# Performance work log

Hardware: AMD Instinct MI355X
Metric: run time of the kernel (lower is better)

The kernel has to match this reference:

```python
import jax, jax.numpy as jnp
import numpy as np

N_NODES = 50000
N_EDGES = 800000
N_GRAPHS = 128
IN_DIM, HID_DIM, OUT_DIM = 128, 96, 10


def setup_inputs() -> dict:
    key = jax.random.key(0)
    ks = jax.random.split(key, 9)
    x = jax.random.normal(ks[0], (N_NODES, IN_DIM), dtype=jnp.float32)
    edge_index = jax.random.randint(ks[1], (2, N_EDGES), 0, N_NODES, dtype=jnp.int32)
    batch = jnp.sort(jax.random.randint(ks[2], (N_NODES,), 0, N_GRAPHS, dtype=jnp.int32))
    s1 = 1.0 / np.sqrt(IN_DIM)
    s2 = 1.0 / np.sqrt(HID_DIM)
    W1 = jax.random.uniform(ks[3], (IN_DIM, HID_DIM), jnp.float32, -s1, s1)
    b1 = jnp.zeros((HID_DIM,), jnp.float32)
    W2 = jax.random.uniform(ks[4], (HID_DIM, HID_DIM), jnp.float32, -s2, s2)
    b2 = jnp.zeros((HID_DIM,), jnp.float32)
    Wf = jax.random.uniform(ks[5], (OUT_DIM, HID_DIM), jnp.float32, -s2, s2)
    bf = jax.random.uniform(ks[6], (OUT_DIM,), jnp.float32, -s2, s2)
    return {"x": x, "edge_index": edge_index, "batch": batch,
            "W1": W1, "b1": b1, "W2": W2, "b2": b2, "Wf": Wf, "bf": bf}


def reference(x, edge_index, batch, W1, b1, W2, b2, Wf, bf):
    n = x.shape[0]
    row, col = edge_index[0], edge_index[1]
    # GCN symmetric normalization with self-loops: deg = 1 + in-degree
    deg = jax.ops.segment_sum(jnp.ones_like(col, dtype=x.dtype), col, num_segments=n) + 1.0
    dinv = deg ** -0.5  # [N]
    norm = dinv[row] * dinv[col]  # [E]

    def gcn_conv(h, W, b):
        h = h @ W  # [N, F_out]
        # edge messages: norm_e * h[src] scattered to dst; self-loops handled analytically
        agg = jax.ops.segment_sum(norm[:, None] * h[row], col, num_segments=n)
        agg = agg + (dinv * dinv)[:, None] * h
        return agg + b

    h = jax.nn.relu(gcn_conv(x, W1, b1))
    h = gcn_conv(h, W2, b2)

    # global mean pool over graphs
    counts = jax.ops.segment_sum(jnp.ones((n,), x.dtype), batch, num_segments=N_GRAPHS)
    pooled = jax.ops.segment_sum(h, batch, num_segments=N_GRAPHS)
    pooled = pooled / jnp.maximum(counts, 1.0)[:, None]

    logits = pooled @ Wf.T + bf
    return jax.nn.log_softmax(logits, axis=1)
```

## Files before the change

kernel.cpp:

```cpp
#include <hip/hip_runtime.h>
#include <hip/hip_bf16.h>

#define N_GRAPHS 128
#define HID 96
#define OUT_DIM 10
#define CAP 64

typedef __attribute__((ext_vector_type(8))) short short8;
typedef __attribute__((ext_vector_type(4))) float f32x4;
typedef __attribute__((ext_vector_type(2))) float f32x2;

__device__ inline unsigned short f2bf(float f) {
    union { float f; unsigned u; } x;
    x.f = f;
    unsigned r = x.u + 0x7FFFu + ((x.u >> 16) & 1u);
    return (unsigned short)(r >> 16);
}

__device__ inline unsigned char f2fp8(float v) {
    int p = __builtin_amdgcn_cvt_pk_fp8_f32(v, v, 0, false);
    return (unsigned char)(p & 0xff);
}

__device__ inline void unpack16_fp8(uint4 v, float* o) {
    f32x2 a0 = __builtin_amdgcn_cvt_pk_f32_fp8((int)v.x, false);
    f32x2 a1 = __builtin_amdgcn_cvt_pk_f32_fp8((int)v.x, true);
    f32x2 b0 = __builtin_amdgcn_cvt_pk_f32_fp8((int)v.y, false);
    f32x2 b1 = __builtin_amdgcn_cvt_pk_f32_fp8((int)v.y, true);
    f32x2 c0 = __builtin_amdgcn_cvt_pk_f32_fp8((int)v.z, false);
    f32x2 c1 = __builtin_amdgcn_cvt_pk_f32_fp8((int)v.z, true);
    f32x2 d0 = __builtin_amdgcn_cvt_pk_f32_fp8((int)v.w, false);
    f32x2 d1 = __builtin_amdgcn_cvt_pk_f32_fp8((int)v.w, true);
    o[0] = a0.x;  o[1] = a0.y;  o[2] = a1.x;  o[3] = a1.y;
    o[4] = b0.x;  o[5] = b0.y;  o[6] = b1.x;  o[7] = b1.y;
    o[8] = c0.x;  o[9] = c0.y;  o[10] = c1.x; o[11] = c1.y;
    o[12] = d0.x; o[13] = d0.y; o[14] = d1.x; o[15] = d1.y;
}

__global__ __launch_bounds__(256) void fill_kernel(const int* __restrict__ rowi,
                                                   const int* __restrict__ coli,
                                                   int* __restrict__ cnt,
                                                   unsigned short* __restrict__ srcs,
                                                   int E, int N) {
    const int part = blockIdx.x & 7;
    const int chunk = blockIdx.x >> 3;
    const int base = chunk * 2048;
    const int plo = (int)(((long long)N * part) >> 3);
    const int phi = (int)(((long long)N * (part + 1)) >> 3);
#pragma unroll
    for (int it = 0; it < 8; ++it) {
        int e = base + it * 256 + threadIdx.x;
        if (e < E) {
            int c = coli[e];
            if (c >= plo && c < phi) {
                int pos = atomicAdd(&cnt[c], 1);
                if (pos < CAP) srcs[(size_t)c * CAP + pos] = (unsigned short)rowi[e];
            }
        }
    }
}

__global__ __launch_bounds__(256) void gemm1_mfma(const float* __restrict__ X,
                                                  const float* __restrict__ W,
                                                  const int* __restrict__ cnt,
                                                  unsigned char* __restrict__ Tp, int N) {
    constexpr int K = 128;
    constexpr int P = K + 8;
    constexpr int KT = K / 32;
    __shared__ __align__(16) unsigned short Wt[96 * P];
    const int tid = threadIdx.x;
    const int row0 = blockIdx.x * 64;

    for (int idx = tid; idx < K * 96; idx += 256) {
        int k = idx / 96, n = idx - k * 96;
        Wt[n * P + k] = f2bf(W[idx]);
    }
    __syncthreads();

    const int wv = tid >> 6;
    const int lane = tid & 63;
    const int m = lane & 15;
    const int quad = lane >> 4;
    const int row = row0 + wv * 16 + m;

    short8 afrag[KT];
    if (row < N) {
        const float* Xr = X + (size_t)row * K;
#pragma unroll
        for (int t = 0; t < KT; ++t) {
            float4 a0 = *(const float4*)(Xr + t * 32 + quad * 8);
            float4 a1 = *(const float4*)(Xr + t * 32 + quad * 8 + 4);
            short8 a;
            a[0] = (short)f2bf(a0.x); a[1] = (short)f2bf(a0.y);
            a[2] = (short)f2bf(a0.z); a[3] = (short)f2bf(a0.w);
            a[4] = (short)f2bf(a1.x); a[5] = (short)f2bf(a1.y);
            a[6] = (short)f2bf(a1.z); a[7] = (short)f2bf(a1.w);
            afrag[t] = a;
        }
    } else {
#pragma unroll
        for (int t = 0; t < KT; ++t) afrag[t] = short8{0, 0, 0, 0, 0, 0, 0, 0};
    }

    f32x4 acc[6];
#pragma unroll
    for (int nt = 0; nt < 6; ++nt) acc[nt] = f32x4{0.f, 0.f, 0.f, 0.f};
#pragma unroll
    for (int t = 0; t < KT; ++t) {
#pragma unroll
        for (int nt = 0; nt < 6; ++nt) {
            short8 bfrag = *(const short8*)&Wt[(nt * 16 + m) * P + t * 32 + quad * 8];
            acc[nt] = __builtin_amdgcn_mfma_f32_16x16x32_bf16(afrag[t], bfrag, acc[nt], 0, 0, 0);
        }
    }
#pragma unroll
    for (int r = 0; r < 4; ++r) {
        int orow = row0 + wv * 16 + quad * 4 + r;
        if (orow < N) {
            float d = rsqrtf(1.0f + (float)cnt[orow]);
#pragma unroll
            for (int nt = 0; nt < 6; ++nt)
                Tp[(size_t)orow * 96 + nt * 16 + m] = f2fp8(d * acc[nt][r]);
        }
    }
}

__global__ __launch_bounds__(256) void gather1_gemm2(const unsigned char* __restrict__ Tp1,
                                                     const unsigned short* __restrict__ srcs,
                                                     const int* __restrict__ cnt,
                                                     const float* __restrict__ b1,
                                                     const float* __restrict__ W2,
                                                     unsigned char* __restrict__ Tp2, int N) {
    constexpr int PH = 104;
    constexpr int PW = 104;
    __shared__ __align__(16) unsigned short Hs[128 * PH];
    __shared__ __align__(16) unsigned short Wt[96 * PW];
    const int tid = threadIdx.x;
    const int node0 = blockIdx.x * 128;

    for (int idx = tid; idx < 96 * 96; idx += 256) {
        int k = idx / 96, n = idx - k * 96;
        Wt[n * PW + k] = f2bf(W2[idx]);
    }

    const uint4* Trow = (const uint4*)Tp1;
#pragma unroll
    for (int it = 0; it < 3; ++it) {
        int idx = it * 256 + tid;
        int n = idx / 6, j = idx - n * 6;
        int i = node0 + n;
        if (i < N) {
            float acc[16], tmp[16];
            unpack16_fp8(Trow[(size_t)i * 6 + j], acc);
            int ci = cnt[i];
            int e = min(ci, CAP);
            const unsigned short* sp = srcs + (size_t)i * CAP;
            int k = 0;
            for (; k + 4 <= e; k += 4) {
                ushort4 s4 = *(const ushort4*)(sp + k);
                uint4 v0 = Trow[(size_t)s4.x * 6 + j];
                uint4 v1 = Trow[(size_t)s4.y * 6 + j];
                uint4 v2 = Trow[(size_t)s4.z * 6 + j];
                uint4 v3 = Trow[(size_t)s4.w * 6 + j];
                unpack16_fp8(v0, tmp);
#pragma unroll
                for (int l = 0; l < 16; ++l) acc[l] += tmp[l];
                unpack16_fp8(v1, tmp);
#pragma unroll
                for (int l = 0; l < 16; ++l) acc[l] += tmp[l];
                unpack16_fp8(v2, tmp);
#pragma unroll
                for (int l = 0; l < 16; ++l) acc[l] += tmp[l];
                unpack16_fp8(v3, tmp);
#pragma unroll
                for (int l = 0; l < 16; ++l) acc[l] += tmp[l];
            }
            for (; k < e; ++k) {
                unpack16_fp8(Trow[(size_t)sp[k] * 6 + j], tmp);
#pragma unroll
                for (int l = 0; l < 16; ++l) acc[l] += tmp[l];
            }
            float di = rsqrtf(1.0f + (float)ci);
#pragma unroll
            for (int l = 0; l < 16; ++l) {
                float v = fmaxf(di * acc[l] + b1[j * 16 + l], 0.0f);
                Hs[n * PH + j * 16 + l] = f2bf(v);
            }
        } else {
#pragma unroll
            for (int l = 0; l < 16; ++l) Hs[n * PH + j * 16 + l] = 0;
        }
    }
    __syncthreads();

    const int wv = tid >> 6;
    const int lane = tid & 63;
    const int m = lane & 15;
    const int quad = lane >> 4;
#pragma unroll
    for (int half = 0; half < 2; ++half) {
        const int rt = wv + half * 4;
        const int lrow = rt * 16 + m;
        short8 afrag[3];
#pragma unroll
        for (int t = 0; t < 3; ++t)
            afrag[t] = *(const short8*)&Hs[lrow * PH + t * 32 + quad * 8];
        f32x4 acc[6];
#pragma unroll
        for (int nt = 0; nt < 6; ++nt) acc[nt] = f32x4{0.f, 0.f, 0.f, 0.f};
#pragma unroll
        for (int t = 0; t < 3; ++t) {
#pragma unroll
            for (int nt = 0; nt < 6; ++nt) {
                short8 bfrag = *(const short8*)&Wt[(nt * 16 + m) * PW + t * 32 + quad * 8];
                acc[nt] = __builtin_amdgcn_mfma_f32_16x16x32_bf16(afrag[t], bfrag, acc[nt], 0, 0, 0);
            }
        }
#pragma unroll
        for (int r = 0; r < 4; ++r) {
            int orow = node0 + rt * 16 + quad * 4 + r;
            if (orow < N) {
                float d = rsqrtf(1.0f + (float)cnt[orow]);
#pragma unroll
                for (int nt = 0; nt < 6; ++nt)
                    Tp2[(size_t)orow * 96 + nt * 16 + m] = f2fp8(d * acc[nt][r]);
            }
        }
    }
}

__global__ __launch_bounds__(192) void gather2_pool(const unsigned char* __restrict__ Tp,
                                                    const unsigned short* __restrict__ srcs,
                                                    const int* __restrict__ cnt,
                                                    const int* __restrict__ batch,
                                                    float* __restrict__ pooled, int N) {
    __shared__ float hl[32 * 96];
    __shared__ int g_l[32];
    const int tid = threadIdx.x;
    const int n = tid / 6;
    const int j = tid - n * 6;
    const int i = blockIdx.x * 32 + n;
    if (tid < 32) {
        int ii = blockIdx.x * 32 + tid;
        g_l[tid] = (ii < N) ? batch[ii] : -1;
    }

    float acc[16];
#pragma unroll
    for (int l = 0; l < 16; ++l) acc[l] = 0.0f;
    float di = 0.0f;
    if (i < N) {
        const uint4* Trow = (const uint4*)Tp;
        float tmp[16];
        unpack16_fp8(Trow[(size_t)i * 6 + j], acc);
        int ci = cnt[i];
        di = rsqrtf(1.0f + (float)ci);
        int e = min(ci, CAP);
        const unsigned short* sp = srcs + (size_t)i * CAP;
        int k = 0;
        for (; k + 4 <= e; k += 4) {
            ushort4 s4 = *(const ushort4*)(sp + k);
            uint4 v0 = Trow[(size_t)s4.x * 6 + j];
            uint4 v1 = Trow[(size_t)s4.y * 6 + j];
            uint4 v2 = Trow[(size_t)s4.z * 6 + j];
            uint4 v3 = Trow[(size_t)s4.w * 6 + j];
            unpack16_fp8(v0, tmp);
#pragma unroll
            for (int l = 0; l < 16; ++l) acc[l] += tmp[l];
            unpack16_fp8(v1, tmp);
#pragma unroll
            for (int l = 0; l < 16; ++l) acc[l] += tmp[l];
            unpack16_fp8(v2, tmp);
#pragma unroll
            for (int l = 0; l < 16; ++l) acc[l] += tmp[l];
            unpack16_fp8(v3, tmp);
#pragma unroll
            for (int l = 0; l < 16; ++l) acc[l] += tmp[l];
        }
        for (; k < e; ++k) {
            unpack16_fp8(Trow[(size_t)sp[k] * 6 + j], tmp);
#pragma unroll
            for (int l = 0; l < 16; ++l) acc[l] += tmp[l];
        }
    }
#pragma unroll
    for (int l = 0; l < 16; ++l) hl[n * 96 + j * 16 + l] = di * acc[l];
    __syncthreads();

    if (tid < 96) {
        int f = tid;
        float s = 0.0f;
        int gcur = -2;
        for (int nn = 0; nn < 32; ++nn) {
            int g = g_l[nn];
            if (g < 0) continue;
            if (g != gcur) {
                if (gcur >= 0) atomicAdd(&pooled[gcur * 96 + f], s);
                gcur = g;
                s = 0.0f;
            }
            s += hl[nn * 96 + f];
        }
        if (gcur >= 0) atomicAdd(&pooled[gcur * 96 + f], s);
    }
}

__device__ inline int lower_bound_dev(const int* __restrict__ a, int n, int val) {
    int lo = 0, hi = n;
    while (lo < hi) {
        int m = (lo + hi) >> 1;
        if (a[m] < val) lo = m + 1; else hi = m;
    }
    return lo;
}

__global__ void head_kernel(const float* __restrict__ pooled, const int* __restrict__ batch,
                            const float* __restrict__ b2, const float* __restrict__ Wf,
                            const float* __restrict__ bfv, float* __restrict__ out, int N) {
    __shared__ float wfs[OUT_DIM * HID];
    __shared__ float b2s[HID];
    __shared__ float bfs[OUT_DIM];
    int t = threadIdx.x;
    for (int idx = t; idx < OUT_DIM * HID; idx += 128) wfs[idx] = Wf[idx];
    if (t < HID) b2s[t] = b2[t];
    if (t < OUT_DIM) bfs[t] = bfv[t];
    __syncthreads();
    int g = t;
    if (g >= N_GRAPHS) return;
    int lo = lower_bound_dev(batch, N, g);
    int hi = lower_bound_dev(batch, N, g + 1);
    int c = hi - lo;
    float inv = (c > 0) ? 1.0f / (float)c : 0.0f;
    float hasb = (c > 0) ? 1.0f : 0.0f;
    float logits[OUT_DIM];
#pragma unroll
    for (int o = 0; o < OUT_DIM; ++o) {
        float s = 0.0f;
        for (int cc = 0; cc < HID; ++cc)
            s += (pooled[g * HID + cc] * inv + hasb * b2s[cc]) * wfs[o * HID + cc];
        logits[o] = s + bfs[o];
    }
    float m = logits[0];
#pragma unroll
    for (int o = 1; o < OUT_DIM; ++o) m = fmaxf(m, logits[o]);
    float se = 0.0f;
#pragma unroll
    for (int o = 0; o < OUT_DIM; ++o) se += expf(logits[o] - m);
    float lse = m + logf(se);
#pragma unroll
    for (int o = 0; o < OUT_DIM; ++o) out[g * OUT_DIM + o] = logits[o] - lse;
}

extern "C" void kernel_launch(void* const* d_in, const int* in_sizes, int n_in,
                              void* d_out, int out_size, void* d_ws, size_t ws_size,
                              hipStream_t stream) {
    const float* x     = (const float*)d_in[0];
    const int*   ei    = (const int*)d_in[1];
    const int*   batch = (const int*)d_in[2];
    const float* W1    = (const float*)d_in[3];
    const float* b1    = (const float*)d_in[4];
    const float* W2    = (const float*)d_in[5];
    const float* b2    = (const float*)d_in[6];
    const float* Wf    = (const float*)d_in[7];
    const float* bf    = (const float*)d_in[8];

    const int N = in_sizes[0] / 128;
    const int E = in_sizes[1] / 2;
    const int* rowi = ei;
    const int* coli = ei + E;

    size_t off = 0;
    auto alloc = [&](size_t bytes) {
        void* p = (char*)d_ws + off;
        off += (bytes + 255) & ~(size_t)255;
        return p;
    };
    int*            cnt    = (int*)alloc((size_t)N * 4);
    float*          pooled = (float*)alloc((size_t)N_GRAPHS * HID * 4);
    size_t zero_bytes = off;
    unsigned short* srcs   = (unsigned short*)alloc((size_t)N * CAP * 2);
    unsigned char*  Tp1    = (unsigned char*)alloc((size_t)N * HID);
    unsigned char*  Tp2    = (unsigned char*)alloc((size_t)N * HID);

    hipMemsetAsync(d_ws, 0, zero_bytes, stream);

    const int nchunk = (E + 2047) / 2048;
    fill_kernel<<<nchunk * 8, 256, 0, stream>>>(rowi, coli, cnt, srcs, E, N);

    gemm1_mfma<<<(N + 63) / 64, 256, 0, stream>>>(x, W1, cnt, Tp1, N);

    gather1_gemm2<<<(N + 127) / 128, 256, 0, stream>>>(Tp1, srcs, cnt, b1, W2, Tp2, N);

    gather2_pool<<<(N + 31) / 32, 192, 0, stream>>>(Tp2, srcs, cnt, batch, pooled, N);

    head_kernel<<<1, 128, 0, stream>>>(pooled, batch, b2, Wf, bf, (float*)d_out, N);
}
```

Measured before the change: 215.2 us.

## Pad fp8 feature rows to 128 bytes, halve gather tile, count graph sizes via atomics

Feature tables Tp1 and Tp2 now use a 128-byte row stride instead of 96, so every gathered row starts on a cache-line boundary and addressing becomes a shift. gather1_gemm2 processes 64 nodes per block instead of 128, which raises the block count and shrinks shared memory per block. Per-graph node counts are now accumulated with atomics inside fill_kernel, replacing the binary searches in the single-block head kernel. The padding costs extra memory footprint, and the per-node atomics add some contention.

Measured after the change: 319.1 us. 48.2% more time.

```diff
diff --git a/kernel.cpp b/kernel.cpp
--- a/kernel.cpp
+++ b/kernel.cpp
@@ -5,6 +5,7 @@
 #define HID 96
 #define OUT_DIM 10
 #define CAP 64
+#define TROW 128
 
 typedef __attribute__((ext_vector_type(8))) short short8;
 typedef __attribute__((ext_vector_type(4))) float f32x4;
@@ -39,7 +40,9 @@
 
 __global__ __launch_bounds__(256) void fill_kernel(const int* __restrict__ rowi,
                                                    const int* __restrict__ coli,
+                                                   const int* __restrict__ batch,
                                                    int* __restrict__ cnt,
+                                                   int* __restrict__ gcount,
                                                    unsigned short* __restrict__ srcs,
                                                    int E, int N) {
     const int part = blockIdx.x & 7;
@@ -58,6 +61,9 @@
             }
         }
     }
+    const int gstride = gridDim.x * 256;
+    for (int i = blockIdx.x * 256 + threadIdx.x; i < N; i += gstride)
+        atomicAdd(&gcount[batch[i]], 1);
 }
 
 __global__ __launch_bounds__(256) void gemm1_mfma(const float* __restrict__ X,
@@ -120,7 +126,7 @@
             float d = rsqrtf(1.0f + (float)cnt[orow]);
 #pragma unroll
             for (int nt = 0; nt < 6; ++nt)
-                Tp[(size_t)orow * 96 + nt * 16 + m] = f2fp8(d * acc[nt][r]);
+                Tp[(size_t)orow * TROW + nt * 16 + m] = f2fp8(d * acc[nt][r]);
         }
     }
 }
@@ -133,10 +139,10 @@
                                                      unsigned char* __restrict__ Tp2, int N) {
     constexpr int PH = 104;
     constexpr int PW = 104;
-    __shared__ __align__(16) unsigned short Hs[128 * PH];
+    __shared__ __align__(16) unsigned short Hs[64 * PH];
     __shared__ __align__(16) unsigned short Wt[96 * PW];
     const int tid = threadIdx.x;
-    const int node0 = blockIdx.x * 128;
+    const int node0 = blockIdx.x * 64;
 
     for (int idx = tid; idx < 96 * 96; idx += 256) {
         int k = idx / 96, n = idx - k * 96;
@@ -145,50 +151,52 @@
 
     const uint4* Trow = (const uint4*)Tp1;
 #pragma unroll
-    for (int it = 0; it < 3; ++it) {
+    for (int it = 0; it < 2; ++it) {
         int idx = it * 256 + tid;
-        int n = idx / 6, j = idx - n * 6;
-        int i = node0 + n;
-        if (i < N) {
-            float acc[16], tmp[16];
-            unpack16_fp8(Trow[(size_t)i * 6 + j], acc);
-            int ci = cnt[i];
-            int e = min(ci, CAP);
-            const unsigned short* sp = srcs + (size_t)i * CAP;
-            int k = 0;
-            for (; k + 4 <= e; k += 4) {
-                ushort4 s4 = *(const ushort4*)(sp + k);
-                uint4 v0 = Trow[(size_t)s4.x * 6 + j];
-                uint4 v1 = Trow[(size_t)s4.y * 6 + j];
-                uint4 v2 = Trow[(size_t)s4.z * 6 + j];
-                uint4 v3 = Trow[(size_t)s4.w * 6 + j];
-                unpack16_fp8(v0, tmp);
-#pragma unroll
-                for (int l = 0; l < 16; ++l) acc[l] += tmp[l];
-                unpack16_fp8(v1, tmp);
-#pragma unroll
-                for (int l = 0; l < 16; ++l) acc[l] += tmp[l];
-                unpack16_fp8(v2, tmp);
-#pragma unroll
-                for (int l = 0; l < 16; ++l) acc[l] += tmp[l];
-                unpack16_fp8(v3, tmp);
-#pragma unroll
-                for (int l = 0; l < 16; ++l) acc[l] += tmp[l];
+        if (idx < 384) {
+            int n = idx / 6, j = idx - n * 6;
+            int i = node0 + n;
+            if (i < N) {
+                float acc[16], tmp[16];
+                unpack16_fp8(Trow[((size_t)i << 3) + j], acc);
+                int ci = cnt[i];
+                int e = min(ci, CAP);
+                const unsigned short* sp = srcs + (size_t)i * CAP;
+                int k = 0;
+                for (; k + 4 <= e; k += 4) {
+                    ushort4 s4 = *(const ushort4*)(sp + k);
+                    uint4 v0 = Trow[((size_t)s4.x << 3) + j];
+                    uint4 v1 = Trow[((size_t)s4.y << 3) + j];
+                    uint4 v2 = Trow[((size_t)s4.z << 3) + j];
+                    uint4 v3 = Trow[((size_t)s4.w << 3) + j];
+                    unpack16_fp8(v0, tmp);
+#pragma unroll
+                    for (int l = 0; l < 16; ++l) acc[l] += tmp[l];
+                    unpack16_fp8(v1, tmp);
+#pragma unroll
+                    for (int l = 0; l < 16; ++l) acc[l] += tmp[l];
+                    unpack16_fp8(v2, tmp);
+#pragma unroll
+                    for (int l = 0; l < 16; ++l) acc[l] += tmp[l];
+                    unpack16_fp8(v3, tmp);
+#pragma unroll
+                    for (int l = 0; l < 16; ++l) acc[l] += tmp[l];
+                }
+                for (; k < e; ++k) {
+                    unpack16_fp8(Trow[((size_t)sp[k] << 3) + j], tmp);
+#pragma unroll
+                    for (int l = 0; l < 16; ++l) acc[l] += tmp[l];
+                }
+                float di = rsqrtf(1.0f + (float)ci);
+#pragma unroll
+                for (int l = 0; l < 16; ++l) {
+                    float v = fmaxf(di * acc[l] + b1[j * 16 + l], 0.0f);
+                    Hs[n * PH + j * 16 + l] = f2bf(v);
+                }
+            } else {
+#pragma unroll
+                for (int l = 0; l < 16; ++l) Hs[n * PH + j * 16 + l] = 0;
             }
-            for (; k < e; ++k) {
-                unpack16_fp8(Trow[(size_t)sp[k] * 6 + j], tmp);
-#pragma unroll
-                for (int l = 0; l < 16; ++l) acc[l] += tmp[l];
-            }
-            float di = rsqrtf(1.0f + (float)ci);
-#pragma unroll
-            for (int l = 0; l < 16; ++l) {
-                float v = fmaxf(di * acc[l] + b1[j * 16 + l], 0.0f);
-                Hs[n * PH + j * 16 + l] = f2bf(v);
-            }
-        } else {
-#pragma unroll
-            for (int l = 0; l < 16; ++l) Hs[n * PH + j * 16 + l] = 0;
         }
     }
     __syncthreads();
@@ -197,34 +205,30 @@
     const int lane = tid & 63;
     const int m = lane & 15;
     const int quad = lane >> 4;
-#pragma unroll
-    for (int half = 0; half < 2; ++half) {
-        const int rt = wv + half * 4;
-        const int lrow = rt * 16 + m;
-        short8 afrag[3];
-#pragma unroll
-        for (int t = 0; t < 3; ++t)
-            afrag[t] = *(const short8*)&Hs[lrow * PH + t * 32 + quad * 8];
-        f32x4 acc[6];
-#pragma unroll
-        for (int nt = 0; nt < 6; ++nt) acc[nt] = f32x4{0.f, 0.f, 0.f, 0.f};
-#pragma unroll
-        for (int t = 0; t < 3; ++t) {
-#pragma unroll
-            for (int nt = 0; nt < 6; ++nt) {
-                short8 bfrag = *(const short8*)&Wt[(nt * 16 + m) * PW + t * 32 + quad * 8];
-                acc[nt] = __builtin_amdgcn_mfma_f32_16x16x32_bf16(afrag[t], bfrag, acc[nt], 0, 0, 0);
-            }
-        }
-#pragma unroll
-        for (int r = 0; r < 4; ++r) {
-            int orow = node0 + rt * 16 + quad * 4 + r;
-            if (orow < N) {
-                float d = rsqrtf(1.0f + (float)cnt[orow]);
-#pragma unroll
-                for (int nt = 0; nt < 6; ++nt)
-                    Tp2[(size_t)orow * 96 + nt * 16 + m] = f2fp8(d * acc[nt][r]);
-            }
+    const int lrow = wv * 16 + m;
+    short8 afrag[3];
+#pragma unroll
+    for (int t = 0; t < 3; ++t)
+        afrag[t] = *(const short8*)&Hs[lrow * PH + t * 32 + quad * 8];
+    f32x4 acc[6];
+#pragma unroll
+    for (int nt = 0; nt < 6; ++nt) acc[nt] = f32x4{0.f, 0.f, 0.f, 0.f};
+#pragma unroll
+    for (int t = 0; t < 3; ++t) {
+#pragma unroll
+        for (int nt = 0; nt < 6; ++nt) {
+            short8 bfrag = *(const short8*)&Wt[(nt * 16 + m) * PW + t * 32 + quad * 8];
+            acc[nt] = __builtin_amdgcn_mfma_f32_16x16x32_bf16(afrag[t], bfrag, acc[nt], 0, 0, 0);
+        }
+    }
+#pragma unroll
+    for (int r = 0; r < 4; ++r) {
+        int orow = node0 + wv * 16 + quad * 4 + r;
+        if (orow < N) {
+            float d = rsqrtf(1.0f + (float)cnt[orow]);
+#pragma unroll
+            for (int nt = 0; nt < 6; ++nt)
+                Tp2[(size_t)orow * TROW + nt * 16 + m] = f2fp8(d * acc[nt][r]);
         }
     }
 }
@@ -252,7 +256,7 @@
     if (i < N) {
         const uint4* Trow = (const uint4*)Tp;
         float tmp[16];
-        unpack16_fp8(Trow[(size_t)i * 6 + j], acc);
+        unpack16_fp8(Trow[((size_t)i << 3) + j], acc);
         int ci = cnt[i];
         di = rsqrtf(1.0f + (float)ci);
         int e = min(ci, CAP);
@@ -260,10 +264,10 @@
         int k = 0;
         for (; k + 4 <= e; k += 4) {
             ushort4 s4 = *(const ushort4*)(sp + k);
-            uint4 v0 = Trow[(size_t)s4.x * 6 + j];
-            uint4 v1 = Trow[(size_t)s4.y * 6 + j];
-            uint4 v2 = Trow[(size_t)s4.z * 6 + j];
-            uint4 v3 = Trow[(size_t)s4.w * 6 + j];
+            uint4 v0 = Trow[((size_t)s4.x << 3) + j];
+            uint4 v1 = Trow[((size_t)s4.y << 3) + j];
+            uint4 v2 = Trow[((size_t)s4.z << 3) + j];
+            uint4 v3 = Trow[((size_t)s4.w << 3) + j];
             unpack16_fp8(v0, tmp);
 #pragma unroll
             for (int l = 0; l < 16; ++l) acc[l] += tmp[l];
@@ -278,7 +282,7 @@
             for (int l = 0; l < 16; ++l) acc[l] += tmp[l];
         }
         for (; k < e; ++k) {
-            unpack16_fp8(Trow[(size_t)sp[k] * 6 + j], tmp);
+            unpack16_fp8(Trow[((size_t)sp[k] << 3) + j], tmp);
 #pragma unroll
             for (int l = 0; l < 16; ++l) acc[l] += tmp[l];
         }
@@ -305,18 +309,9 @@
     }
 }
 
-__device__ inline int lower_bound_dev(const int* __restrict__ a, int n, int val) {
-    int lo = 0, hi = n;
-    while (lo < hi) {
-        int m = (lo + hi) >> 1;
-        if (a[m] < val) lo = m + 1; else hi = m;
-    }
-    return lo;
-}
-
-__global__ void head_kernel(const float* __restrict__ pooled, const int* __restrict__ batch,
+__global__ void head_kernel(const float* __restrict__ pooled, const int* __restrict__ gcount,
                             const float* __restrict__ b2, const float* __restrict__ Wf,
-                            const float* __restrict__ bfv, float* __restrict__ out, int N) {
+                            const float* __restrict__ bfv, float* __restrict__ out) {
     __shared__ float wfs[OUT_DIM * HID];
     __shared__ float b2s[HID];
     __shared__ float bfs[OUT_DIM];
@@ -327,9 +322,7 @@
     __syncthreads();
     int g = t;
     if (g >= N_GRAPHS) return;
-    int lo = lower_bound_dev(batch, N, g);
-    int hi = lower_bound_dev(batch, N, g + 1);
-    int c = hi - lo;
+    int c = gcount[g];
     float inv = (c > 0) ? 1.0f / (float)c : 0.0f;
     float hasb = (c > 0) ? 1.0f : 0.0f;
     float logits[OUT_DIM];
@@ -377,21 +370,22 @@
     };
     int*            cnt    = (int*)alloc((size_t)N * 4);
     float*          pooled = (float*)alloc((size_t)N_GRAPHS * HID * 4);
+    int*            gcount = (int*)alloc((size_t)N_GRAPHS * 4);
     size_t zero_bytes = off;
     unsigned short* srcs   = (unsigned short*)alloc((size_t)N * CAP * 2);
-    unsigned char*  Tp1    = (unsigned char*)alloc((size_t)N * HID);
-    unsigned char*  Tp2    = (unsigned char*)alloc((size_t)N * HID);
+    unsigned char*  Tp1    = (unsigned char*)alloc((size_t)N * TROW);
+    unsigned char*  Tp2    = (unsigned char*)alloc((size_t)N * TROW);
 
     hipMemsetAsync(d_ws, 0, zero_bytes, stream);
 
     const int nchunk = (E + 2047) / 2048;
-    fill_kernel<<<nchunk * 8, 256, 0, stream>>>(rowi, coli, cnt, srcs, E, N);
+    fill_kernel<<<nchunk * 8, 256, 0, stream>>>(rowi, coli, batch, cnt, gcount, srcs, E, N);
 
     gemm1_mfma<<<(N + 63) / 64, 256, 0, stream>>>(x, W1, cnt, Tp1, N);
 
-    gather1_gemm2<<<(N + 127) / 128, 256, 0, stream>>>(Tp1, srcs, cnt, b1, W2, Tp2, N);
+    gather1_gemm2<<<(N + 63) / 64, 256, 0, stream>>>(Tp1, srcs, cnt, b1, W2, Tp2, N);
 
     gather2_pool<<<(N + 31) / 32, 192, 0, stream>>>(Tp2, srcs, cnt, batch, pooled, N);
 
-    head_kernel<<<1, 128, 0, stream>>>(pooled, batch, b2, Wf, bf, (float*)d_out, N);
-}
+    head_kernel<<<1, 128, 0, stream>>>(pooled, gcount, b2, Wf, bf, (float*)d_out);
+}
```
